# Kernel optimization log

Hardware: AMD Instinct MI355X
Metric: run time of the kernel (lower is better)

## Reference

```python
import jax, jax.numpy as jnp
import numpy as np

P, Q = 8, 8  # patch_size


def _patchify(x):
    # x: [b, c, H, W] -> patches [b, h*w, c*p*q]
    b, c, H, W = x.shape
    h, w = H // P, W // Q
    x = x.reshape(b, c, h, P, w, Q)
    x = x.transpose(0, 2, 4, 1, 3, 5)  # b h w c p q
    return x.reshape(b, h * w, c * P * Q)


def _depatchify(patches, c, H, W):
    # patches: [b, h*w, c*p*q] -> [b, c, H, W]
    b = patches.shape[0]
    h, w = H // P, W // Q
    x = patches.reshape(b, h, w, c, P, Q)
    x = x.transpose(0, 3, 1, 4, 2, 5)  # b c h p w q
    return x.reshape(b, c, H, W)


def setup_inputs() -> dict:
    key = jax.random.key(0)
    x = jax.random.normal(key, (16, 3, 512, 512), dtype=jnp.float32)
    return {"x": x, "rank": 32}


def reference(x, rank):
    b, c, H, W = x.shape
    patches = _patchify(x)  # [b, N, D] with N = (H/8)*(W/8), D = c*64
    u, s, vt = jnp.linalg.svd(patches, full_matrices=False)
    u = u[..., :rank]          # [b, N, r]
    s = s[..., :rank]          # [b, r]
    vt = vt[..., :rank, :]     # [b, r, D]
    # original: u*sqrt(s), v = sqrt(s)*vt^T; reconstruction u @ v^T == (u*s) @ vt
    recon = (u * s[..., None, :]) @ vt  # [b, N, D]
    return _depatchify(recon, c, H, W)
```

## Files before the change

### kernel.cpp

```cpp
#include <hip/hip_runtime.h>
#include <cstdint>
#include <cstddef>

#define IMG 512
#define JD 192

__device__ inline float fast_rcp(float x) { return __builtin_amdgcn_rcpf(x); }

__global__ __launch_bounds__(512) void k_gram(const float* __restrict__ x,
                                              float* __restrict__ part) {
  const int ck = blockIdx.x;
  const int sl = blockIdx.y;
  const int b  = blockIdx.z;
  const int t  = threadIdx.x;
  __shared__ float tile[32][JD];
  const int ty = t >> 5;
  const int tx = t & 31;
  const int r0 = sl*48 + ty*3;
  const int c0 = tx*6;
  float acc[3][6];
#pragma unroll
  for (int i=0;i<3;i++)
#pragma unroll
    for (int j=0;j<6;j++) acc[i][j]=0.f;
  const float* xb = x + (size_t)b*3*IMG*IMG;
  const int nbeg = ck*1024;
  for (int n0 = nbeg; n0 < nbeg+1024; n0 += 32) {
    for (int f = t; f < 32*JD; f += 512) {
      const int nl = f / JD, j = f - nl*JD;
      const int n = n0 + nl;
      const int hh = n >> 6, ww = n & 63;
      const int c = j >> 6, p = (j >> 3) & 7, q = j & 7;
      tile[nl][j] = xb[(c*IMG + hh*8+p)*IMG + ww*8 + q];
    }
    __syncthreads();
#pragma unroll 4
    for (int nl = 0; nl < 32; nl++) {
      float va[3], vb[6];
#pragma unroll
      for (int i=0;i<3;i++) va[i] = tile[nl][r0+i];
#pragma unroll
      for (int j=0;j<6;j++) vb[j] = tile[nl][c0+j];
#pragma unroll
      for (int i=0;i<3;i++)
#pragma unroll
        for (int j=0;j<6;j++) acc[i][j] += va[i]*vb[j];
    }
    __syncthreads();
  }
  float* dst = part + (((size_t)(b*4 + sl))*4 + ck) * (size_t)(48*JD);
#pragma unroll
  for (int i=0;i<3;i++)
#pragma unroll
    for (int j=0;j<6;j++)
      dst[(ty*3+i)*JD + c0+j] = acc[i][j];
}

__global__ __launch_bounds__(256) void k_greduce(const float* __restrict__ part,
                                                 float* __restrict__ Gs) {
  const int idx = blockIdx.x*256 + threadIdx.x;
  const int b = idx / (JD*JD);
  const int e = idx - b*(JD*JD);
  const int r = e / JD;
  const int sl = r / 48;
  const int w = (r - sl*48)*JD + (e - r*JD);
  const float* p = part + ((size_t)(b*4+sl))*4*(48*JD) + w;
  float s = 0.f;
#pragma unroll
  for (int ck=0; ck<4; ck++) s += p[(size_t)ck*48*JD];
  Gs[idx] = s * (1.0f/4096.0f);
}

__global__ __launch_bounds__(512) void k_sq(const float* __restrict__ S,
                                            float* __restrict__ D) {
  const int tp = blockIdx.x;
  const int b  = blockIdx.y;
  int ti, tj;
  if      (tp==0){ti=0;tj=0;} else if (tp==1){ti=1;tj=0;}
  else if (tp==2){ti=1;tj=1;} else if (tp==3){ti=2;tj=0;}
  else if (tp==4){ti=2;tj=1;} else            {ti=2;tj=2;}
  const float* Sb = S + (size_t)b*JD*JD;
  float* Db = D + (size_t)b*JD*JD;
  __shared__ float Ar[64][33];
  __shared__ float Br[64][33];
  const int t = threadIdx.x;
  const int ty = t >> 4, tx = t & 15;
  float acc[2][4];
#pragma unroll
  for (int i=0;i<2;i++)
#pragma unroll
    for (int j=0;j<4;j++) acc[i][j]=0.f;
  for (int k0=0; k0<JD; k0+=32) {
    for (int f=t; f<2048; f+=512) {
      const int row = f >> 5, kk = f & 31;
      Ar[row][kk] = Sb[(ti*64+row)*JD + k0+kk];
      Br[row][kk] = Sb[(tj*64+row)*JD + k0+kk];
    }
    __syncthreads();
#pragma unroll 4
    for (int k=0;k<32;k++) {
      float va[2], vb[4];
#pragma unroll
      for (int i=0;i<2;i++) va[i] = Ar[ty*2+i][k];
#pragma unroll
      for (int j=0;j<4;j++) vb[j] = Br[tx*4+j][k];
#pragma unroll
      for (int i=0;i<2;i++)
#pragma unroll
        for (int j=0;j<4;j++) acc[i][j] += va[i]*vb[j];
    }
    __syncthreads();
  }
#pragma unroll
  for (int i=0;i<2;i++)
#pragma unroll
    for (int j=0;j<4;j++) {
      const int r = ti*64+ty*2+i, c = tj*64+tx*4+j;
      Db[r*JD+c] = acc[i][j];
      if (ti != tj) Db[c*JD+r] = acc[i][j];
    }
}


__device__ void orth_lds(float* __restrict__ Wl, float* __restrict__ S1,
                         float* __restrict__ rdv, float* __restrict__ pdv,
                         float* __restrict__ misc, int t, float ridge) {
  const int ty = t >> 5, tx = t & 31;
  float acc[4][2];
#pragma unroll
  for (int i=0;i<4;i++)
#pragma unroll
    for (int j=0;j<2;j++) acc[i][j]=0.f;
  __syncthreads();
#pragma unroll 2
  for (int r=0; r<JD; r++) {
    const float4 va4 = *(const float4*)(Wl + r*68 + ty*4);
    const float2 vb2 = *(const float2*)(Wl + r*68 + tx*2);
    const float a4[4] = {va4.x, va4.y, va4.z, va4.w};
    const float b2[2] = {vb2.x, vb2.y};
#pragma unroll
    for (int i=0;i<4;i++)
#pragma unroll
      for (int j=0;j<2;j++) acc[i][j] += a4[i]*b2[j];
  }
#pragma unroll
  for (int i=0;i<4;i++)
#pragma unroll
    for (int j=0;j<2;j++)
      S1[(ty*4+i)*68 + tx*2+j] = acc[i][j];
  __syncthreads();
  if (ridge > 0.f) {
    if (t < 64) {
      float d = S1[t*68+t];
#pragma unroll
      for (int o=1;o<64;o<<=1) d = fmaxf(d, __shfl_xor(d, o));
      if (t == 0) misc[0] = d * ridge;
    }
    __syncthreads();
    if (t < 64) S1[t*68+t] += misc[0];
    __syncthreads();
  }
  for (int p=0; p<4; p++) {
    const int b16 = p*16;
    if (t < 64) {
      for (int jj=0; jj<16; jj++) {
        const int j = b16 + jj;
        const float invd = fast_rcp(S1[j*68+j]);
        if (t == 0) pdv[jj] = invd;
        const int nit = (15-jj)*16;
        for (int f=t; f<nit; f+=64) {
          const int i = j+1 + (f>>4);
          const int k = j+1 + (f&15);
          if (k <= i)
            S1[i*68+k] -= S1[i*68+j]*S1[k*68+j]*invd;
        }
      }
    }
    __syncthreads();
    const int rb = b16 + 16;
    if (t < 64 - rb) {
      const int r = rb + t;
      float pr[16];
      float4* prp = (float4*)pr;
      prp[0] = *(const float4*)(S1 + r*68 + b16);
      prp[1] = *(const float4*)(S1 + r*68 + b16 + 4);
      prp[2] = *(const float4*)(S1 + r*68 + b16 + 8);
      prp[3] = *(const float4*)(S1 + r*68 + b16 + 12);
#pragma unroll
      for (int c=1; c<16; c++) {
        float s = pr[c];
#pragma unroll
        for (int j=0; j<c; j++) s -= pr[j]*S1[(b16+c)*68 + b16+j]*pdv[j];
        pr[c] = s;
      }
      *(float4*)(S1 + r*68 + b16)      = prp[0];
      *(float4*)(S1 + r*68 + b16 + 4)  = prp[1];
      *(float4*)(S1 + r*68 + b16 + 8)  = prp[2];
      *(float4*)(S1 + r*68 + b16 + 12) = prp[3];
    }
    __syncthreads();
    for (int f=t; f<2304; f+=512) {
      const int i = rb + f/48;
      const int k = rb + (f - (f/48)*48);
      if (i < 64 && k < 64 && k <= i) {
        float s = S1[i*68+k];
#pragma unroll
        for (int jj=0; jj<16; jj++)
          s -= S1[i*68 + b16+jj]*S1[k*68 + b16+jj]*pdv[jj];
        S1[i*68+k] = s;
      }
    }
    __syncthreads();
  }
  if (t < 64) rdv[t] = rsqrtf(S1[t*68+t]);
  __syncthreads();
  for (int f=t; f<4096; f+=512) {
    const int i = f>>6, k = f&63;
    if (k < i) S1[i*68+k] *= rdv[k];
  }
  __syncthreads();
  if (t < JD) {
    float w[64];
    float4* wp = (float4*)w;
#pragma unroll
    for (int c4=0;c4<16;c4++) wp[c4] = *(const float4*)(Wl + t*68 + c4*4);
#pragma unroll
    for (int c=0;c<64;c++) {
      float v = w[c];
#pragma unroll
      for (int k=0;k<c;k++) v -= w[k]*S1[c*68+k];
      w[c] = v * rdv[c];
    }
#pragma unroll
    for (int c4=0;c4<16;c4++) *(float4*)(Wl + t*68 + c4*4) = wp[c4];
  }
  __syncthreads();
}

__device__ void mm_lds(const float* __restrict__ G, const float* __restrict__ Win,
                       float* __restrict__ Wout, float* __restrict__ Gt, int t) {
  const int rg = t >> 3;
  const int cg = t & 7;
  float acc[3][8];
#pragma unroll
  for (int i=0;i<3;i++)
#pragma unroll
    for (int j=0;j<8;j++) acc[i][j]=0.f;
  for (int k0=0; k0<JD; k0+=32) {
    __syncthreads();
    for (int f=t; f<6144; f+=512) {
      const int r = f >> 5, kk = f & 31;
      Gt[kk*193 + r] = G[r*JD + k0 + kk];
    }
    __syncthreads();
#pragma unroll 2
    for (int k=0;k<32;k++) {
      const float a0 = Gt[k*193 + rg*3+0];
      const float a1 = Gt[k*193 + rg*3+1];
      const float a2 = Gt[k*193 + rg*3+2];
      const float* wr = Win + (k0+k)*68 + cg*8;
#pragma unroll
      for (int j4=0;j4<2;j4++) {
        const float4 b4 = *(const float4*)(wr + 4*j4);
        const float bb[4] = {b4.x, b4.y, b4.z, b4.w};
#pragma unroll
        for (int jj=0;jj<4;jj++) {
          acc[0][j4*4+jj] += a0*bb[jj];
          acc[1][j4*4+jj] += a1*bb[jj];
          acc[2][j4*4+jj] += a2*bb[jj];
        }
      }
    }
  }
  __syncthreads();
#pragma unroll
  for (int i=0;i<3;i++)
#pragma unroll
    for (int j=0;j<8;j++)
      Wout[(rg*3+i)*68 + cg*8 + j] = acc[i][j];
  __syncthreads();
}

__device__ void hgemm_lds(const float* __restrict__ X, const float* __restrict__ Y,
                          float* __restrict__ S1, int ss, int t) {
  const int ty = t >> 5, tx = t & 31;
  float acc[4][2];
#pragma unroll
  for (int i=0;i<4;i++)
#pragma unroll
    for (int j=0;j<2;j++) acc[i][j]=0.f;
#pragma unroll 2
  for (int r=0; r<JD; r++) {
    const float4 va4 = *(const float4*)(X + r*68 + ty*4);
    const float2 vb2 = *(const float2*)(Y + r*68 + tx*2);
    const float a4[4] = {va4.x, va4.y, va4.z, va4.w};
    const float b2[2] = {vb2.x, vb2.y};
#pragma unroll
    for (int i=0;i<4;i++)
#pragma unroll
      for (int j=0;j<2;j++) acc[i][j] += a4[i]*b2[j];
  }
  __syncthreads();
#pragma unroll
  for (int i=0;i<4;i++)
#pragma unroll
    for (int j=0;j<2;j++)
      S1[(ty*4+i)*ss + tx*2+j] = acc[i][j];
  __syncthreads();
}

__global__ __launch_bounds__(512) void k_subH(const float* __restrict__ G32g,
                                              const float* __restrict__ Gsg,
                                              float* __restrict__ WbG,
                                              float* __restrict__ Hgg) {
  const int b = blockIdx.x;
  const int t = threadIdx.x;
  __shared__ float W0l[192*68];
  __shared__ float W1l[192*68];
  __shared__ float scr[32*193];
  __shared__ float rdv[64];
  __shared__ float pdv[16];
  __shared__ float misc[8];
  const float* Gb  = G32g + (size_t)b*JD*JD;
  const float* Gsb = Gsg  + (size_t)b*JD*JD;

  for (int f=t; f<JD*64; f+=512)
    W0l[(f>>6)*68 + (f&63)] = Gb[(f>>6)*JD + (f&63)];
  __syncthreads();

  orth_lds(W0l, scr, rdv, pdv, misc, t, 1e-6f);
  mm_lds(Gb, W0l, W1l, scr, t);
  orth_lds(W1l, scr, rdv, pdv, misc, t, 1e-6f);
  orth_lds(W1l, scr, rdv, pdv, misc, t, 0.f);

  mm_lds(Gsb, W1l, W0l, scr, t);
  hgemm_lds(W1l, W0l, scr, 65, t);

  float* Wb = WbG + (size_t)b*JD*64;
  for (int f=t; f<JD*64; f+=512)
    Wb[f] = W1l[(f>>6)*68 + (f&63)];
  float* Hb = Hgg + (size_t)b*4160;
  for (int f=t; f<4160; f+=512) Hb[f] = scr[f];
}

__device__ void dev_tridiag(float* __restrict__ A, float* a, float* b2,
                            float* bsg, float* v0s, float* bts,
                            float* vvec, float* wvec, int t) {
  for (int j=0; j<=61; j++) {
    const int m = 63 - j;
    if (t < 64) {
      float xi = (t < m) ? A[j*65 + (j+1+t)] : 0.f;
      float nr = xi*xi;
#pragma unroll
      for (int o=1;o<64;o<<=1) nr += __shfl_xor(nr, o);
      const float sig = sqrtf(nr);
      const float alpha = __shfl(xi, 0);
      const float sgn = (alpha >= 0.f) ? 1.f : -1.f;
      const float v0 = alpha + sgn*sig;
      const float beta = (sig > 1e-20f) ? 1.0f/(sig*fabsf(v0)) : 0.f;
      if (t < m) vvec[t] = (t==0) ? v0 : xi;
      if (t == 0) {
        a[j] = A[j*65+j]; b2[j] = nr; bsg[j] = -sgn*sig;
        v0s[j] = v0; bts[j] = beta;
      }
      float pv = 0.f;
      if (t < m) {
        const float* row = A + (j+1+t)*65 + (j+1);
        for (int c=0;c<m;c++) pv += row[c]*vvec[c];
        pv *= beta;
      }
      float dp = (t<m) ? vvec[t]*pv : 0.f;
#pragma unroll
      for (int o=1;o<64;o<<=1) dp += __shfl_xor(dp, o);
      const float gamma = 0.5f*beta*dp;
      if (t < m) wvec[t] = pv - gamma*vvec[t];
    }
    __syncthreads();
    const int mm = m*m;
    for (int f=t; f<mm; f+=256) {
      const int r = f/m, c = f - r*m;
      A[(j+1+r)*65 + (j+1+c)] -= vvec[r]*wvec[c] + wvec[r]*vvec[c];
    }
    __syncthreads();
  }
  if (t == 0) {
    a[62] = A[62*65+62];
    a[63] = A[63*65+63];
    const float bb = A[62*65+63];
    b2[62] = bb*bb;
    bsg[62] = bb;
  }
  __syncthreads();
}

__device__ inline int sturm_cnt_fast(const float* a, const float* b2, float sig) {
  float d = a[0] - sig;
  int n = (d < 0.f) ? 1 : 0;
#pragma unroll 8
  for (int i=1;i<64;i++) {
    const float dd = (fabsf(d) < 1e-20f) ? -1e-20f : d;
    d = (a[i]-sig) - b2[i-1]*fast_rcp(dd);
    n += (d < 0.f) ? 1 : 0;
  }
  return n;
}

__device__ inline float dguard(float d) {
  if (fabsf(d) < 1e-12f) return (d < 0.f) ? -1e-12f : 1e-12f;
  return d;
}

__global__ __launch_bounds__(256) void k_eigv(const float* __restrict__ Hgg,
                                              float* __restrict__ VtG) {
  const int b = blockIdx.x;
  const int t = threadIdx.x;
  __shared__ float SH[4160];
  __shared__ float Vt[64*36];
  __shared__ float dpA[64*33];
  __shared__ float dmA[64*33];
  __shared__ float ps[8*33];
  __shared__ float wvred[32];
  __shared__ float rdv[64];
  __shared__ float a64[64];
  __shared__ float b2v[64];
  __shared__ float bsg[64];
  __shared__ float v0s[64];
  __shared__ float bts[64];
  __shared__ float vvec[64];
  __shared__ float wvec[64];
  __shared__ float lam[32];
  __shared__ float misc[8];
  const float* Hb = Hgg + (size_t)b*4160;
  for (int f=t; f<4160; f+=256) SH[f] = Hb[f];
  __syncthreads();

  dev_tridiag(SH, a64, b2v, bsg, v0s, bts, vvec, wvec, t);

  if (t < 64) {
    const float bl = (t>0)  ? sqrtf(b2v[t-1]) : 0.f;
    const float br = (t<63) ? sqrtf(b2v[t])   : 0.f;
    float lo = a64[t] - bl - br, hi = a64[t] + bl + br;
#pragma unroll
    for (int o=1;o<64;o<<=1) {
      lo = fminf(lo, __shfl_xor(lo,o));
      hi = fmaxf(hi, __shfl_xor(hi,o));
    }
    if (t == 0) { misc[0] = lo - 1e-4f; misc[1] = hi + 1e-4f; }
  }
  __syncthreads();

  {
    const int l = t >> 3, g = t & 7;
    const int r = 32 + l;
    float L = misc[0], H = misc[1];
    for (int it=0; it<10; it++) {
      const float mid = L + (H-L)*((float)(g+1)*(1.0f/9.0f));
      const int cnt = sturm_cnt_fast(a64, b2v, mid);
      float nL = L, nH = H;
#pragma unroll
      for (int k=0;k<8;k++) {
        const int ck = __shfl(cnt, k, 8);
        const float pk = L + (H-L)*((float)(k+1)*(1.0f/9.0f));
        if (ck <= r) nL = fmaxf(nL, pk); else nH = fminf(nH, pk);
      }
      L = nL; H = nH;
    }
    if (g == 0) lam[l] = 0.5f*(L+H);
  }
  __syncthreads();

  if (t < 32) {
    const int l = t;
    const float lm = lam[l];
    float d = dguard(a64[0] - lm);
    dpA[0*33+l] = d;
    for (int i=1;i<64;i++) {
      d = dguard((a64[i]-lm) - b2v[i-1]*fast_rcp(d));
      dpA[i*33+l] = d;
    }
    float e = dguard(a64[63] - lm);
    dmA[63*33+l] = e;
    for (int i=62;i>=0;i--) {
      e = dguard((a64[i]-lm) - b2v[i]*fast_rcp(e));
      dmA[i*33+l] = e;
    }
    int ks = 0; float gbest = 1e30f;
    for (int i=0;i<64;i++) {
      const float g = fabsf(dpA[i*33+l] + dmA[i*33+l] - (a64[i]-lm));
      if (g < gbest) { gbest = g; ks = i; }
    }
    Vt[ks*36+l] = 1.f;
    float z = 1.f;
    for (int i=ks-1;i>=0;i--) {
      z = -(bsg[i]*z) * fast_rcp(dpA[i*33+l]);
      z = fminf(fmaxf(z, -1e18f), 1e18f);
      Vt[i*36+l] = z;
    }
    z = 1.f;
    for (int i=ks+1;i<64;i++) {
      z = -(bsg[i-1]*z) * fast_rcp(dmA[i*33+l]);
      z = fminf(fmaxf(z, -1e18f), 1e18f);
      Vt[i*36+l] = z;
    }
    float nr2 = 0.f;
    for (int i=0;i<64;i++) { const float zz = Vt[i*36+l]; nr2 += zz*zz; }
    const float inv = rsqrtf(nr2);
    for (int i=0;i<64;i++) Vt[i*36+l] *= inv;
  }
  __syncthreads();

  for (int f=t; f<1024; f+=256) {
    const int i = f>>5, j = f&31;
    float s = 0.f;
    for (int r=0;r<64;r++) s += Vt[r*36+i]*Vt[r*36+j];
    dpA[i*33+j] = s;
  }
  __syncthreads();
  if (t == 0) {
    float m = 0.f;
    for (int j=0;j<32;j++) m = fmaxf(m, dpA[j*33+j]);
    misc[2] = m * 1e-7f;
  }
  __syncthreads();
  if (t < 32) dpA[t*33+t] += misc[2];
  for (int j=0;j<31;j++) {
    __syncthreads();
    const float invd = fast_rcp(dpA[j*33+j]);
    for (int f=t; f<(31-j)*32; f+=256) {
      const int i = j+1 + (f>>5);
      const int k = f & 31;
      if (k > j && k <= i)
        dpA[i*33+k] -= dpA[i*33+j]*dpA[k*33+j]*invd;
    }
  }
  __syncthreads();
  if (t < 32) rdv[t] = rsqrtf(dpA[t*33+t]);
  __syncthreads();
  for (int f=t; f<1024; f+=256) {
    const int i = f>>5, k = f&31;
    if (k < i) dpA[i*33+k] *= rdv[k];
  }
  __syncthreads();
  if (t < 64) {
    float w[32];
#pragma unroll
    for (int c=0;c<32;c++) w[c] = Vt[t*36+c];
#pragma unroll
    for (int c=0;c<32;c++) {
      float v = w[c];
#pragma unroll
      for (int k=0;k<c;k++) v -= w[k]*dpA[c*33+k];
      w[c] = v * rdv[c];
    }
#pragma unroll
    for (int c=0;c<32;c++) Vt[t*36+c] = w[c];
  }
  __syncthreads();

  for (int j=61; j>=0; j--) {
    const int m = 63 - j;
    {
      const int c = t & 31, g = t >> 5;
      float s = 0.f;
      for (int r=g; r<m; r+=8) {
        const float vr = (r==0) ? v0s[j] : SH[j*65 + (j+1+r)];
        s += vr * Vt[(j+1+r)*36 + c];
      }
      ps[g*33+c] = s;
    }
    __syncthreads();
    if (t < 32) {
      float s = 0.f;
#pragma unroll
      for (int g=0;g<8;g++) s += ps[g*33+t];
      wvred[t] = s * bts[j];
    }
    __syncthreads();
    {
      const int c = t & 31, g = t >> 5;
      for (int r=g; r<m; r+=8) {
        const float vr = (r==0) ? v0s[j] : SH[j*65 + (j+1+r)];
        Vt[(j+1+r)*36 + c] -= vr * wvred[c];
      }
    }
    __syncthreads();
  }

  float* Vb = VtG + (size_t)b*2048;
  for (int f=t; f<2048; f+=256) Vb[f] = Vt[(f>>5)*36 + (f&31)];
}

__global__ __launch_bounds__(256) void k_bv(const float* __restrict__ WbG,
                                            const float* __restrict__ VtG,
                                            float* __restrict__ Btg) {
  const int b = blockIdx.x;
  const int t = threadIdx.x;
  __shared__ float Vt[64*36];
  const float* W = WbG + (size_t)b*JD*64;
  const float* Vb = VtG + (size_t)b*2048;
  float* Bt = Btg + (size_t)b*32*JD;
  for (int f=t; f<2048; f+=256) Vt[(f>>5)*36 + (f&31)] = Vb[f];
  __syncthreads();
  if (t < JD) {
    float accv[32];
#pragma unroll
    for (int c=0;c<32;c++) accv[c] = 0.f;
    const float4* crow = (const float4*)(W + t*64);
#pragma unroll 2
    for (int kb=0; kb<16; kb++) {
      const float4 av = crow[kb];
      const float a4[4] = {av.x, av.y, av.z, av.w};
#pragma unroll
      for (int ki=0; ki<4; ki++) {
        const float aa = a4[ki];
        const float* vrow = Vt + (kb*4+ki)*36;
        const float4 v0 = *(const float4*)(vrow+0);
        const float4 v1 = *(const float4*)(vrow+4);
        const float4 v2 = *(const float4*)(vrow+8);
        const float4 v3 = *(const float4*)(vrow+12);
        const float4 v4 = *(const float4*)(vrow+16);
        const float4 v5 = *(const float4*)(vrow+20);
        const float4 v6 = *(const float4*)(vrow+24);
        const float4 v7 = *(const float4*)(vrow+28);
        accv[0]+=aa*v0.x; accv[1]+=aa*v0.y; accv[2]+=aa*v0.z; accv[3]+=aa*v0.w;
        accv[4]+=aa*v1.x; accv[5]+=aa*v1.y; accv[6]+=aa*v1.z; accv[7]+=aa*v1.w;
        accv[8]+=aa*v2.x; accv[9]+=aa*v2.y; accv[10]+=aa*v2.z; accv[11]+=aa*v2.w;
        accv[12]+=aa*v3.x; accv[13]+=aa*v3.y; accv[14]+=aa*v3.z; accv[15]+=aa*v3.w;
        accv[16]+=aa*v4.x; accv[17]+=aa*v4.y; accv[18]+=aa*v4.z; accv[19]+=aa*v4.w;
        accv[20]+=aa*v5.x; accv[21]+=aa*v5.y; accv[22]+=aa*v5.z; accv[23]+=aa*v5.w;
        accv[24]+=aa*v6.x; accv[25]+=aa*v6.y; accv[26]+=aa*v6.z; accv[27]+=aa*v6.w;
        accv[28]+=aa*v7.x; accv[29]+=aa*v7.y; accv[30]+=aa*v7.z; accv[31]+=aa*v7.w;
      }
    }
#pragma unroll
    for (int c=0;c<32;c++) Bt[c*JD + t] = accv[c];
  }
}

__global__ __launch_bounds__(256) void k_mm(const float* __restrict__ Btg,
                                            float* __restrict__ Mg) {
  const int tp = blockIdx.x;
  const int b  = blockIdx.y;
  int ti, tj;
  if      (tp==0){ti=0;tj=0;} else if (tp==1){ti=1;tj=0;}
  else if (tp==2){ti=1;tj=1;} else if (tp==3){ti=2;tj=0;}
  else if (tp==4){ti=2;tj=1;} else            {ti=2;tj=2;}
  const float* Bt = Btg + (size_t)b*32*JD;
  float* Mb = Mg + (size_t)b*JD*JD;
  __shared__ float Ar[32][68];
  __shared__ float Br[32][68];
  const int t = threadIdx.x;
  const int ty = t >> 4, tx = t & 15;
  for (int f=t; f<2048; f+=256) {
    const int k = f >> 6, c = f & 63;
    Ar[k][c] = Bt[k*JD + ti*64 + c];
    Br[k][c] = Bt[k*JD + tj*64 + c];
  }
  __syncthreads();
  float acc[4][4];
#pragma unroll
  for (int i=0;i<4;i++)
#pragma unroll
    for (int j=0;j<4;j++) acc[i][j]=0.f;
#pragma unroll 4
  for (int k=0;k<32;k++) {
    const float4 va4 = *(const float4*)(&Ar[k][ty*4]);
    const float4 vb4 = *(const float4*)(&Br[k][tx*4]);
    const float a4[4] = {va4.x, va4.y, va4.z, va4.w};
    const float b4[4] = {vb4.x, vb4.y, vb4.z, vb4.w};
#pragma unroll
    for (int i=0;i<4;i++)
#pragma unroll
      for (int j=0;j<4;j++) acc[i][j] += a4[i]*b4[j];
  }
#pragma unroll
  for (int i=0;i<4;i++)
#pragma unroll
    for (int j=0;j<4;j++) {
      const int r = ti*64+ty*4+i, c = tj*64+tx*4+j;
      Mb[r*JD+c] = acc[i][j];
      if (ti != tj) Mb[c*JD+r] = acc[i][j];
    }
}

__global__ __launch_bounds__(256) void k_recon(const float* __restrict__ x,
                                               const float* __restrict__ Mg,
                                               float* __restrict__ out) {
  const int nb = blockIdx.x;
  const int b  = blockIdx.y;
  const int t  = threadIdx.x;
  __shared__ float At[32][17];
  __shared__ float Mt[16][JD];
  const float* xb = x + (size_t)b*3*IMG*IMG;
  const float* Mb = Mg + (size_t)b*JD*JD;
  float* ob = out + (size_t)b*3*IMG*IMG;
  const int pg = t >> 4;
  const int jg = t & 15;
  float acc[2][12];
#pragma unroll
  for (int i=0;i<2;i++)
#pragma unroll
    for (int j=0;j<12;j++) acc[i][j]=0.f;
  for (int j0=0; j0<JD; j0+=16) {
    for (int f=t; f<512; f+=256) {
      const int nl = f >> 4, jj = f & 15;
      const int j = j0 + jj;
      const int n = nb*32 + nl;
      const int hh = n >> 6, ww = n & 63;
      const int c = j >> 6, p = (j >> 3) & 7, q = j & 7;
      At[nl][jj] = xb[(c*IMG + hh*8+p)*IMG + ww*8 + q];
    }
    for (int f=t; f<768; f+=256) {
      const int jj = f/48, cc = (f - jj*48)*4;
      *(float4*)(&Mt[jj][cc]) = *(const float4*)(Mb + (size_t)(j0+jj)*JD + cc);
    }
    __syncthreads();
#pragma unroll 4
    for (int jj=0;jj<16;jj++) {
      const float a0 = At[pg*2+0][jj];
      const float a1 = At[pg*2+1][jj];
      const float4 m0 = *(const float4*)(&Mt[jj][jg*12]);
      const float4 m1 = *(const float4*)(&Mt[jj][jg*12+4]);
      const float4 m2 = *(const float4*)(&Mt[jj][jg*12+8]);
      const float mm[12] = {m0.x,m0.y,m0.z,m0.w,m1.x,m1.y,m1.z,m1.w,
                            m2.x,m2.y,m2.z,m2.w};
#pragma unroll
      for (int j=0;j<12;j++) {
        acc[0][j] += a0*mm[j];
        acc[1][j] += a1*mm[j];
      }
    }
    __syncthreads();
  }
#pragma unroll
  for (int i=0;i<2;i++) {
    const int n = nb*32 + pg*2 + i;
    const int hh = n >> 6, ww = n & 63;
#pragma unroll
    for (int j4=0;j4<3;j4++) {
      const int jo = jg*12 + j4*4;
      const int c = jo >> 6, p = (jo >> 3) & 7, q = jo & 7;
      const float4 v = make_float4(acc[i][j4*4+0], acc[i][j4*4+1],
                                   acc[i][j4*4+2], acc[i][j4*4+3]);
      *(float4*)(ob + (size_t)(c*IMG + hh*8+p)*IMG + ww*8 + q) = v;
    }
  }
}

extern "C" void kernel_launch(void* const* d_in, const int* in_sizes, int n_in,
                              void* d_out, int out_size, void* d_ws, size_t ws_size,
                              hipStream_t stream) {
  (void)in_sizes; (void)n_in; (void)out_size; (void)ws_size;
  const float* x = (const float*)d_in[0];
  float* out = (float*)d_out;
  float* ws  = (float*)d_ws;

  float* part = ws;
  float* Gs   = ws + 2359296;
  float* P0   = ws + 2949120;
  float* P1   = ws + 3538944;
  float* Mg   = ws;
  float* Wb   = ws + 786432;
  float* Hg   = ws + 983040;
  float* Vtg  = ws + 1057792;
  float* Btg  = ws + 1090560;

  k_gram  <<<dim3(4,4,16), 512, 0, stream>>>(x, part);
  k_greduce<<<2304,        256, 0, stream>>>(part, Gs);
  k_sq    <<<dim3(6,16),   512, 0, stream>>>(Gs, P0);
  k_sq    <<<dim3(6,16),   512, 0, stream>>>(P0, P1);
  k_sq    <<<dim3(6,16),   512, 0, stream>>>(P1, P0);
  k_sq    <<<dim3(6,16),   512, 0, stream>>>(P0, P1);
  k_sq    <<<dim3(6,16),   512, 0, stream>>>(P1, P0);
  k_subH  <<<16,           512, 0, stream>>>(P0, Gs, Wb, Hg);
  k_eigv  <<<16,           256, 0, stream>>>(Hg, Vtg);
  k_bv    <<<16,           256, 0, stream>>>(Wb, Vtg, Btg);
  k_mm    <<<dim3(6,16),   256, 0, stream>>>(Btg, Mg);
  k_recon <<<dim3(128,16), 256, 0, stream>>>(x, Mg, out);
}
```

Measured before the change: 944.0 us.

## Enlarge register tiles in gram and squaring kernels, split gram K across thread groups

The gram kernel now gives each thread a 6x6 output tile and uses float2 LDS loads. The two 256-thread halves of the block each take half of the 32 rows in every tile and are summed through shared memory at the end. The squaring kernel drops to 256 threads with a 4x4 tile per thread. The aim is more FMAs per LDS load, with higher register use and an extra shared-memory reduction pass in exchange.

```diff
diff --git a/kernel.cpp b/kernel.cpp
--- a/kernel.cpp
+++ b/kernel.cpp
@@ -14,17 +14,21 @@
   const int b  = blockIdx.z;
   const int t  = threadIdx.x;
   __shared__ float tile[32][JD];
-  const int ty = t >> 5;
-  const int tx = t & 31;
-  const int r0 = sl*48 + ty*3;
+  __shared__ float pacc[256*37];
+  const int g   = t >> 8;
+  const int tid = t & 255;
+  const int ty = tid >> 5;
+  const int tx = tid & 31;
+  const int r0 = sl*48 + ty*6;
   const int c0 = tx*6;
-  float acc[3][6];
-#pragma unroll
-  for (int i=0;i<3;i++)
+  float acc[6][6];
+#pragma unroll
+  for (int i=0;i<6;i++)
 #pragma unroll
     for (int j=0;j<6;j++) acc[i][j]=0.f;
   const float* xb = x + (size_t)b*3*IMG*IMG;
   const int nbeg = ck*1024;
+  const int nlo = g*16, nhi = nlo+16;
   for (int n0 = nbeg; n0 < nbeg+1024; n0 += 32) {
     for (int f = t; f < 32*JD; f += 512) {
       const int nl = f / JD, j = f - nl*JD;
@@ -35,25 +39,37 @@
     }
     __syncthreads();
 #pragma unroll 4
-    for (int nl = 0; nl < 32; nl++) {
-      float va[3], vb[6];
-#pragma unroll
-      for (int i=0;i<3;i++) va[i] = tile[nl][r0+i];
-#pragma unroll
-      for (int j=0;j<6;j++) vb[j] = tile[nl][c0+j];
-#pragma unroll
-      for (int i=0;i<3;i++)
+    for (int nl = nlo; nl < nhi; nl++) {
+      const float2 a01 = *(const float2*)(&tile[nl][r0]);
+      const float2 a23 = *(const float2*)(&tile[nl][r0+2]);
+      const float2 a45 = *(const float2*)(&tile[nl][r0+4]);
+      const float2 b01 = *(const float2*)(&tile[nl][c0]);
+      const float2 b23 = *(const float2*)(&tile[nl][c0+2]);
+      const float2 b45 = *(const float2*)(&tile[nl][c0+4]);
+      const float va[6] = {a01.x,a01.y,a23.x,a23.y,a45.x,a45.y};
+      const float vb[6] = {b01.x,b01.y,b23.x,b23.y,b45.x,b45.y};
+#pragma unroll
+      for (int i=0;i<6;i++)
 #pragma unroll
         for (int j=0;j<6;j++) acc[i][j] += va[i]*vb[j];
     }
     __syncthreads();
   }
-  float* dst = part + (((size_t)(b*4 + sl))*4 + ck) * (size_t)(48*JD);
-#pragma unroll
-  for (int i=0;i<3;i++)
-#pragma unroll
-    for (int j=0;j<6;j++)
-      dst[(ty*3+i)*JD + c0+j] = acc[i][j];
+  if (g == 1) {
+#pragma unroll
+    for (int i=0;i<6;i++)
+#pragma unroll
+      for (int j=0;j<6;j++) pacc[tid*37 + i*6+j] = acc[i][j];
+  }
+  __syncthreads();
+  if (g == 0) {
+    float* dst = part + (((size_t)(b*4 + sl))*4 + ck) * (size_t)(48*JD);
+#pragma unroll
+    for (int i=0;i<6;i++)
+#pragma unroll
+      for (int j=0;j<6;j++)
+        dst[(ty*6+i)*JD + c0+j] = acc[i][j] + pacc[tid*37 + i*6+j];
+  }
 }
 
 __global__ __launch_bounds__(256) void k_greduce(const float* __restrict__ part,
@@ -71,7 +87,7 @@
   Gs[idx] = s * (1.0f/4096.0f);
 }
 
-__global__ __launch_bounds__(512) void k_sq(const float* __restrict__ S,
+__global__ __launch_bounds__(256) void k_sq(const float* __restrict__ S,
                                             float* __restrict__ D) {
   const int tp = blockIdx.x;
   const int b  = blockIdx.y;
@@ -85,13 +101,13 @@
   __shared__ float Br[64][33];
   const int t = threadIdx.x;
   const int ty = t >> 4, tx = t & 15;
-  float acc[2][4];
-#pragma unroll
-  for (int i=0;i<2;i++)
+  float acc[4][4];
+#pragma unroll
+  for (int i=0;i<4;i++)
 #pragma unroll
     for (int j=0;j<4;j++) acc[i][j]=0.f;
   for (int k0=0; k0<JD; k0+=32) {
-    for (int f=t; f<2048; f+=512) {
+    for (int f=t; f<2048; f+=256) {
       const int row = f >> 5, kk = f & 31;
       Ar[row][kk] = Sb[(ti*64+row)*JD + k0+kk];
       Br[row][kk] = Sb[(tj*64+row)*JD + k0+kk];
@@ -99,23 +115,23 @@
     __syncthreads();
 #pragma unroll 4
     for (int k=0;k<32;k++) {
-      float va[2], vb[4];
-#pragma unroll
-      for (int i=0;i<2;i++) va[i] = Ar[ty*2+i][k];
+      float va[4], vb[4];
+#pragma unroll
+      for (int i=0;i<4;i++) va[i] = Ar[ty*4+i][k];
 #pragma unroll
       for (int j=0;j<4;j++) vb[j] = Br[tx*4+j][k];
 #pragma unroll
-      for (int i=0;i<2;i++)
+      for (int i=0;i<4;i++)
 #pragma unroll
         for (int j=0;j<4;j++) acc[i][j] += va[i]*vb[j];
     }
     __syncthreads();
   }
 #pragma unroll
-  for (int i=0;i<2;i++)
+  for (int i=0;i<4;i++)
 #pragma unroll
     for (int j=0;j<4;j++) {
-      const int r = ti*64+ty*2+i, c = tj*64+tx*4+j;
+      const int r = ti*64+ty*4+i, c = tj*64+tx*4+j;
       Db[r*JD+c] = acc[i][j];
       if (ti != tj) Db[c*JD+r] = acc[i][j];
     }
@@ -767,11 +783,11 @@
 
   k_gram  <<<dim3(4,4,16), 512, 0, stream>>>(x, part);
   k_greduce<<<2304,        256, 0, stream>>>(part, Gs);
-  k_sq    <<<dim3(6,16),   512, 0, stream>>>(Gs, P0);
-  k_sq    <<<dim3(6,16),   512, 0, stream>>>(P0, P1);
-  k_sq    <<<dim3(6,16),   512, 0, stream>>>(P1, P0);
-  k_sq    <<<dim3(6,16),   512, 0, stream>>>(P0, P1);
-  k_sq    <<<dim3(6,16),   512, 0, stream>>>(P1, P0);
+  k_sq    <<<dim3(6,16),   256, 0, stream>>>(Gs, P0);
+  k_sq    <<<dim3(6,16),   256, 0, stream>>>(P0, P1);
+  k_sq    <<<dim3(6,16),   256, 0, stream>>>(P1, P0);
+  k_sq    <<<dim3(6,16),   256, 0, stream>>>(P0, P1);
+  k_sq    <<<dim3(6,16),   256, 0, stream>>>(P1, P0);
   k_subH  <<<16,           512, 0, stream>>>(P0, Gs, Wb, Hg);
   k_eigv  <<<16,           256, 0, stream>>>(Hg, Vtg);
   k_bv    <<<16,           256, 0, stream>>>(Wb, Vtg, Btg);
```

Result: no change. 953.8 us (+1.0%).
